# Kernel tuning notes

Measured on AMD Instinct MI355X. Metric: run time of the kernel, lower is better.

Reference implementation:

```python
import jax, jax.numpy as jnp
import numpy as np

T, B = 1024, 128
IDIM, CDIM, N, M = 256, 512, 128, 64


def setup_inputs() -> dict:
    key = jax.random.key(0)
    ks = jax.random.split(key, 10)
    stdev = 5.0 / np.sqrt(IDIM + M + CDIM)  # matches _reset_controller
    u = lambda k, shp: jax.random.uniform(k, shp, jnp.float32, -stdev, stdev)
    return {
        "embs": jax.random.normal(ks[0], (T, B, IDIM), jnp.float32),
        "ilen": T // 2,
        # LSTM controller params (PyTorch layout: [4*cdim, in] / [4*cdim, cdim])
        "w_ih": u(ks[1], (4 * CDIM, IDIM + M)),
        "w_hh": u(ks[2], (4 * CDIM, CDIM)),
        "b_ih": jnp.zeros((4 * CDIM,), jnp.float32),
        "b_hh": jnp.zeros((4 * CDIM,), jnp.float32),
        "h0": jax.random.normal(ks[3], (CDIM,), jnp.float32) * 0.05,
        "c0": jax.random.normal(ks[4], (CDIM,), jnp.float32) * 0.05,
        "r0": jax.random.normal(ks[5], (1, M), jnp.float32) * 0.02,
        # memory head params (concrete subclass): write address / write value / read address
        "W_wa": jax.random.normal(ks[6], (N, CDIM), jnp.float32) * 0.02,
        "b_wa": jnp.zeros((N,), jnp.float32),
        "W_wv": jax.random.normal(ks[7], (M, IDIM), jnp.float32) * 0.02,
        "b_wv": jnp.zeros((M,), jnp.float32),
        "W_ra": jax.random.normal(ks[8], (N, CDIM), jnp.float32) * 0.02,
        "b_ra": jnp.zeros((N,), jnp.float32),
    }


def _forward(embs, w_ih, w_hh, b_ih, b_hh, h0, c0, r0,
             W_wa, b_wa, W_wv, b_wv, W_ra, b_ra, ilen):
    bsz = embs.shape[1]
    h = jnp.broadcast_to(h0, (bsz, CDIM))
    c = jnp.broadcast_to(c0, (bsz, CDIM))
    r = jnp.broadcast_to(r0, (bsz, M))
    mem = jnp.zeros((bsz, N, M), embs.dtype)
    b = b_ih + b_hh

    def step(carry, xt):
        h, c, r, mem = carry
        emb, t = xt  # emb: [B, idim]
        x = jnp.concatenate([emb, r], axis=-1)            # [B, idim+M]
        gates = x @ w_ih.T + h @ w_hh.T + b               # [B, 4*cdim]
        i, f, g, o = jnp.split(gates, 4, axis=-1)         # torch gate order i,f,g,o
        c_new = jax.nn.sigmoid(f) * c + jax.nn.sigmoid(i) * jnp.tanh(g)
        h_new = jax.nn.sigmoid(o) * jnp.tanh(c_new)       # controller_outp
        is_write = t < ilen
        # write(controller_outp, emb): additive write at softmax address
        wa = jax.nn.softmax(h_new @ W_wa.T + b_wa, axis=-1)   # [B, N]
        v = emb @ W_wv.T + b_wv                               # [B, M]
        mem_new = jnp.where(is_write, mem + wa[:, :, None] * v[:, None, :], mem)
        # read(controller_outp): softmax-addressed weighted sum over slots
        ra = jax.nn.softmax(h_new @ W_ra.T + b_ra, axis=-1)   # [B, N]
        r_read = jnp.einsum('bn,bnm->bm', ra, mem_new)        # [B, M]
        r_new = jnp.where(is_write, r, r_read)
        out = jnp.concatenate([h_new, r_new], axis=-1)        # [B, cdim+M]
        return (h_new, c_new, r_new, mem_new), out

    _, os = jax.lax.scan(step, (h, c, r, mem),
                         (embs, jnp.arange(embs.shape[0])))
    return os  # [T, B, cdim+M]


def reference(embs, ilen, w_ih, w_hh, b_ih, b_hh, h0, c0, r0,
              W_wa, b_wa, W_wv, b_wv, W_ra, b_ra):
    return _forward(embs, w_ih, w_hh, b_ih, b_hh, h0, c0, r0,
                    W_wa, b_wa, W_wv, b_wv, W_ra, b_ra, ilen)
```

## Files before the change

### kernel.cpp

```cpp
#include <hip/hip_runtime.h>

typedef _Float16 f16;
typedef __attribute__((ext_vector_type(8))) _Float16 half8;
typedef __attribute__((ext_vector_type(2))) _Float16 half2v;
typedef __attribute__((ext_vector_type(4))) float f32x4;
typedef __attribute__((ext_vector_type(4))) unsigned int u32x4;
typedef unsigned long long u64;

#define TSTEPS 1024

static const size_t OFF_WP   = 0;
static const size_t OFF_BIAS = 3407872;
static const size_t OFF_EMBP = 3416064;
static const size_t OFF_V    = 70524928;
static const size_t OFF_XPRH = 104079360;
static const size_t OFF_MEM  = 104374272;
static const size_t OFF_BAR  = 108568576;
static const size_t OFF_WVP  = 108569600;
static const size_t WS_NEED  = 108602368;


__global__ void marnn_packw(const float* __restrict__ w_ih, const float* __restrict__ w_hh,
                            const float* __restrict__ b_ih, const float* __restrict__ b_hh,
                            f16* __restrict__ WP, float* __restrict__ biasP) {
  int idx = blockIdx.x * 256 + threadIdx.x;
  if (idx < 2048) {
    int j = idx >> 2, g = idx & 3, rg = g * 512 + j;
    biasP[idx] = b_ih[rg] + b_hh[rg];
  }
  if (idx >= 1703936) return;
  int e = idx & 7, l = (idx >> 3) & 63;
  int q = idx >> 9;
  int ks = q % 26; int ntile = q / 26;
  int n = ntile * 16 + (l & 15);
  int k = ks * 32 + (l >> 4) * 8 + e;
  int j2 = n >> 2, g2 = n & 3, rg2 = g2 * 512 + j2;
  float v = (k < 320) ? w_ih[(size_t)rg2 * 320 + k] : w_hh[(size_t)rg2 * 512 + (k - 320)];
  WP[idx] = (f16)v;
}

__global__ void marnn_packwv(const float* __restrict__ W_wv, f16* __restrict__ WVP) {
  int idx = blockIdx.x * 256 + threadIdx.x;
  if (idx >= 16384) return;
  int e = idx & 7, l = (idx >> 3) & 63, ks = (idx >> 9) & 7, nt = idx >> 12;
  int n = nt * 16 + (l & 15);
  int k = ks * 32 + (l >> 4) * 8 + e;
  WVP[idx] = (f16)W_wv[n * 256 + k];
}

__global__ void marnn_packemb(const float* __restrict__ embs, f16* __restrict__ embsP) {
  const long total8 = (long)1024 * 128 * 32;
  const long stride = (long)gridDim.x * blockDim.x;
  for (long i8 = (long)blockIdx.x * blockDim.x + threadIdx.x; i8 < total8; i8 += stride) {
    int bl = (int)(i8 & 15), kc = (int)((i8 >> 4) & 31), bg = (int)((i8 >> 9) & 7);
    long t = i8 >> 12;
    const float* s = embs + ((t * 128) + bg * 16 + bl) * 256 + kc * 8;
    f32x4 a = *(const f32x4*)s, b = *(const f32x4*)(s + 4);
    half8 h;
    h[0]=(f16)a[0]; h[1]=(f16)a[1]; h[2]=(f16)a[2]; h[3]=(f16)a[3];
    h[4]=(f16)b[0]; h[5]=(f16)b[1]; h[6]=(f16)b[2]; h[7]=(f16)b[3];
    *(half8*)(embsP + i8 * 8) = h;
  }
}

__global__ __launch_bounds__(256)
void marnn_vpre(const f16* __restrict__ embsP, const f16* __restrict__ WVP,
                const float* __restrict__ b_wv, float* __restrict__ V) {
  const int tb = blockIdx.x;
  const int wv = threadIdx.x >> 6, l = threadIdx.x & 63;
  half8 bf[8];
  #pragma unroll
  for (int ks = 0; ks < 8; ++ks)
    bf[ks] = *(const half8*)(WVP + ((size_t)(wv * 8 + ks) * 64 + l) * 8);
  const f16* ab = embsP + (size_t)tb * 4096;
  f32x4 acc = {0.f, 0.f, 0.f, 0.f};
  #pragma unroll
  for (int ks = 0; ks < 8; ++ks) {
    half8 af = *(const half8*)(ab + ((size_t)(ks * 4 + (l >> 4)) * 16 + (l & 15)) * 8);
    acc = __builtin_amdgcn_mfma_f32_16x16x32_f16(bf[ks], af, acc, 0, 0, 0);
  }
  const int b = (tb & 7) * 16 + (l & 15);
  const long t = tb >> 3;
  #pragma unroll
  for (int r = 0; r < 4; ++r) {
    int m = wv * 16 + (l >> 4) * 4 + r;
    V[((t * 128) + b) * 64 + m] = acc[r] + b_wv[m];
  }
}

__global__ void marnn_init(const float* __restrict__ h0, const float* __restrict__ r0,
                           f16* __restrict__ XPRH) {
  int idx = blockIdx.x * 256 + threadIdx.x;
  if (idx >= 147456) return;
  int e = idx & 7; int q = idx >> 7; int kcidx = q % 72;
  float v = (kcidx < 8) ? r0[kcidx * 8 + e] : h0[(kcidx - 8) * 8 + e];
  XPRH[idx] = (f16)v;
}


struct __align__(16) MarnnSMem {
  f16  whead[128 * 512];
  char xl[26624];
  char un[4096];
};

__device__ __forceinline__ float marnn_dot8(half8 a, half8 b, float acc) {
#if __has_builtin(__builtin_amdgcn_fdot2)
  half2v a0 = {a[0],a[1]}, a1 = {a[2],a[3]}, a2 = {a[4],a[5]}, a3 = {a[6],a[7]};
  half2v b0 = {b[0],b[1]}, b1 = {b[2],b[3]}, b2 = {b[4],b[5]}, b3 = {b[6],b[7]};
  acc = __builtin_amdgcn_fdot2(a0, b0, acc, false);
  acc = __builtin_amdgcn_fdot2(a1, b1, acc, false);
  acc = __builtin_amdgcn_fdot2(a2, b2, acc, false);
  acc = __builtin_amdgcn_fdot2(a3, b3, acc, false);
#else
  #pragma unroll
  for (int e = 0; e < 8; ++e) acc += (float)a[e] * (float)b[e];
#endif
  return acc;
}

__device__ __forceinline__ float fast_sigmoid(float x) {
  return __builtin_amdgcn_rcpf(1.f + __expf(-x));
}
__device__ __forceinline__ float fast_tanh(float x) {
  return 1.f - 2.f * __builtin_amdgcn_rcpf(1.f + __expf(2.f * x));
}

__device__ __forceinline__ unsigned ld_flag(const unsigned* p) {
  return __hip_atomic_load(p, __ATOMIC_RELAXED, __HIP_MEMORY_SCOPE_AGENT);
}
__device__ __forceinline__ void st_flag(unsigned* p, unsigned v) {
  __hip_atomic_store(p, v, __ATOMIC_RELAXED, __HIP_MEMORY_SCOPE_AGENT);
}
__device__ __forceinline__ u64 ld_llc64(const void* p) {
  return __hip_atomic_load((const u64*)p, __ATOMIC_RELAXED, __HIP_MEMORY_SCOPE_AGENT);
}
__device__ __forceinline__ void st_llc32(void* p, unsigned v) {
  __hip_atomic_store((unsigned*)p, v, __ATOMIC_RELAXED, __HIP_MEMORY_SCOPE_AGENT);
}

__device__ __forceinline__ void poll16(const unsigned* line, unsigned ep) {
  int l = threadIdx.x & 63;
  for (;;) {
    unsigned v = (l < 16) ? ld_flag(line + l) : ep;
    if (__all((int)(v >= ep))) break;
    __builtin_amdgcn_s_sleep(1);
  }
  asm volatile("" ::: "memory");
}

union H2U { f16 f; unsigned short u; };

__global__ __launch_bounds__(512, 1)
void marnn_main(const int* __restrict__ ilen_p, const float* __restrict__ c0,
                const float* __restrict__ r0,
                const float* __restrict__ W_wa, const float* __restrict__ b_wa,
                const float* __restrict__ W_ra, const float* __restrict__ b_ra,
                float* __restrict__ out, char* __restrict__ ws) {
  __shared__ MarnnSMem sm;

  const f16*   WP    = (const f16*)(ws + OFF_WP);
  const float* biasP = (const float*)(ws + OFF_BIAS);
  const f16*   embsP = (const f16*)(ws + OFF_EMBP);
  const float* Vbuf  = (const float*)(ws + OFF_V);
  f16*         XPRH  = (f16*)(ws + OFF_XPRH);
  float*       MEMB  = (float*)(ws + OFF_MEM);
  unsigned*    FLAGS = (unsigned*)(ws + OFF_BAR);

  const int blk = blockIdx.x, tid = threadIdx.x;
  const int wav = tid >> 6, lane = tid & 63;
  const int g = blk & 7, ns = blk >> 3;
  const int ilen = ilen_p[0];
  unsigned* gfh = FLAGS + g * 32;
  unsigned* gfr = gfh + 16;

  half8 bfr[26];
  {
    const f16* wpb = WP + ((size_t)(ns * 8 + wav) * 26) * 512 + lane * 8;
    #pragma unroll
    for (int ks = 0; ks < 26; ++ks) bfr[ks] = *(const half8*)(wpb + ks * 512);
  }

  auto loadWhead = [&](const float* Wsrc) {
    for (int i = tid; i < 8192; i += 512) {
      int n = i >> 6, slot = i & 63;
      const float* s = Wsrc + n * 512 + slot * 8;
      f32x4 a = *(const f32x4*)(s), b2 = *(const f32x4*)(s + 4);
      half8 hv;
      hv[0]=(f16)a[0]; hv[1]=(f16)a[1]; hv[2]=(f16)a[2]; hv[3]=(f16)a[3];
      hv[4]=(f16)b2[0]; hv[5]=(f16)b2[1]; hv[6]=(f16)b2[2]; hv[7]=(f16)b2[3];
      *(half8*)((char*)sm.whead + (n << 10) + (((slot + n) & 63) << 4)) = hv;
    }
  };
  loadWhead(ilen > 0 ? W_wa : W_ra);

  {
    const u32x4* s0 = (const u32x4*)(embsP + ((size_t)0 * 8 + g) * 4096);
    ((u32x4*)sm.xl)[tid] = s0[tid];
    const u32x4* s1 = (const u32x4*)(XPRH + (((size_t)0 * 8 + g) * 72 + 8) * 128);
    u32x4* d1 = (u32x4*)(sm.xl + 10240);
    d1[tid * 2] = s1[tid * 2]; d1[tid * 2 + 1] = s1[tid * 2 + 1];
  }
  __syncthreads();

  const int b_lane = lane & 15, sel = lane >> 4;
  const int jg = ns * 32 + wav * 4 + sel;
  float c = c0[jg];
  const f32x4 bias4 = *(const f32x4*)(biasP + jg * 4);
  const float r0v = (tid < 64) ? r0[tid] : 0.f;
  const int b = g * 16 + ns;

  const float bw0 = b_wa[lane], bw1 = b_wa[lane + 64];
  const float br0 = b_ra[lane], br1 = b_ra[lane + 64];
  const int gn = (wav & 3) * 32 + (lane & 31);
  const int kq = ((wav >> 2) << 1) | (lane >> 5);

  half8 rf0, rf1;
  #pragma unroll
  for (int e = 0; e < 8; ++e) {
    rf0[e] = (f16)r0[sel * 8 + e];
    rf1[e] = (f16)r0[32 + sel * 8 + e];
  }

  for (int t = 0; t < TSTEPS; ++t) {
    const int par = t & 1, nxt = par ^ 1;
    const bool iswrite = (t < ilen);

    u32x4 sa = {0u, 0u, 0u, 0u};
    if (t + 1 < TSTEPS)
      sa = ((const u32x4*)(embsP + (((size_t)(t + 1) * 8) + g) * 4096))[tid];
    f32x4 vv4 = {0.f, 0.f, 0.f, 0.f};
    if (iswrite && wav == 4 && lane < 16)
      vv4 = *(const f32x4*)(Vbuf + ((size_t)t * 128 + b) * 64 + lane * 4);

    f32x4 acc0 = {0.f, 0.f, 0.f, 0.f}, acc1 = {0.f, 0.f, 0.f, 0.f};
    const char* xb = sm.xl + sel * 256 + b_lane * 16;
    #pragma unroll
    for (int ks = 0; ks < 8; ++ks) {
      half8 af = *(const half8*)(xb + ks * 1024);
      if (ks & 1) acc1 = __builtin_amdgcn_mfma_f32_16x16x32_f16(bfr[ks], af, acc1, 0, 0, 0);
      else        acc0 = __builtin_amdgcn_mfma_f32_16x16x32_f16(bfr[ks], af, acc0, 0, 0, 0);
    }
    #pragma unroll
    for (int ks = 10; ks < 26; ++ks) {
      half8 af = *(const half8*)(xb + ks * 1024);
      if (ks & 1) acc1 = __builtin_amdgcn_mfma_f32_16x16x32_f16(bfr[ks], af, acc1, 0, 0, 0);
      else        acc0 = __builtin_amdgcn_mfma_f32_16x16x32_f16(bfr[ks], af, acc0, 0, 0, 0);
    }
    if (t <= ilen) {
      acc0 = __builtin_amdgcn_mfma_f32_16x16x32_f16(bfr[8], rf0, acc0, 0, 0, 0);
      acc1 = __builtin_amdgcn_mfma_f32_16x16x32_f16(bfr[9], rf1, acc1, 0, 0, 0);
    } else {
      if (wav == 0) {
        poll16(gfr, (unsigned)(t - ilen));
        const u64* rp = (const u64*)(XPRH + (((size_t)par * 8 + g) * 72) * 128
                                     + (lane >> 4) * 128 + (lane & 15) * 8);
        union { u64 u[2]; half8 h; } r0u, r1u;
        r0u.u[0] = ld_llc64(rp);       r0u.u[1] = ld_llc64(rp + 1);
        r1u.u[0] = ld_llc64(rp + 128); r1u.u[1] = ld_llc64(rp + 129);
        char* rdst = sm.xl + 8192 + (lane >> 4) * 256 + (lane & 15) * 16;
        *(half8*)rdst = r0u.h;
        *(half8*)(rdst + 1024) = r1u.h;
      }
      __syncthreads();
      acc0 = __builtin_amdgcn_mfma_f32_16x16x32_f16(bfr[8], *(const half8*)(xb + 8 * 1024), acc0, 0, 0, 0);
      acc1 = __builtin_amdgcn_mfma_f32_16x16x32_f16(bfr[9], *(const half8*)(xb + 9 * 1024), acc1, 0, 0, 0);
    }
    const f32x4 acc = acc0 + acc1;

    {
      float si = fast_sigmoid(acc[0] + bias4[0]);
      float sf = fast_sigmoid(acc[1] + bias4[1]);
      float so = fast_sigmoid(acc[3] + bias4[3]);
      c = sf * c + si * fast_tanh(acc[2] + bias4[2]);
      float h = so * fast_tanh(c);
      H2U cv; cv.f = (f16)h;
      unsigned hu = cv.u;
      unsigned pu = __shfl_down(hu, 16, 64);
      if (!(sel & 1))
        st_llc32(&XPRH[(((size_t)nxt * 8 + g) * 72 + 8 + (jg >> 3)) * 128 + b_lane * 8 + (jg & 7)],
                 hu | (pu << 16));
    }
    asm volatile("s_waitcnt vmcnt(0)" ::: "memory");
    __syncthreads();
    if (tid == 0) st_flag(gfh + ns, (unsigned)(t + 1));
    if (wav == 0) poll16(gfh, (unsigned)(t + 1));
    __syncthreads();

    {
      const u64* s1 = (const u64*)(XPRH + (((size_t)nxt * 8 + g) * 72 + 8) * 128);
      u64 hb0 = ld_llc64(s1 + tid * 4 + 0), hb1 = ld_llc64(s1 + tid * 4 + 1);
      u64 hb2 = ld_llc64(s1 + tid * 4 + 2), hb3 = ld_llc64(s1 + tid * 4 + 3);
      ((u32x4*)sm.xl)[tid] = sa;
      u64* d1 = (u64*)(sm.xl + 10240);
      d1[tid * 4 + 0] = hb0; d1[tid * 4 + 1] = hb1;
      d1[tid * 4 + 2] = hb2; d1[tid * 4 + 3] = hb3;
    }
    __syncthreads();

    {
      int ob = tid >> 5, ojj = tid & 31;
      int oj = ns * 32 + ojj;
      f16 hv = *(const f16*)(sm.xl + 10240 + (oj >> 3) * 256 + ob * 16 + (oj & 7) * 2);
      out[(size_t)t * 73728 + (g * 16 + ob) * 576 + oj] = (float)hv;
    }

    if (t == ilen) { loadWhead(W_ra); __syncthreads(); }
    float* pbuf  = (float*)sm.un;
    float* vpart = (float*)(sm.un + 512);
    float* vred  = (float*)(sm.un + 1536);
    float* vsec  = (float*)(sm.un + 3584);
    {
      if (iswrite && wav == 4 && lane < 16) *(f32x4*)(vsec + lane * 4) = vv4;
      const char* wrow = (const char*)sm.whead + (gn << 10);
      const char* hbase = sm.xl + 10240 + ns * 16;
      float av0 = 0.f, av1 = 0.f;
      #pragma unroll
      for (int i = 0; i < 16; i += 2) {
        int s0 = kq * 16 + i;
        av0 = marnn_dot8(*(const half8*)(wrow + (((s0 + gn) & 63) << 4)),
                         *(const half8*)(hbase + s0 * 256), av0);
        av1 = marnn_dot8(*(const half8*)(wrow + (((s0 + 1 + gn) & 63) << 4)),
                         *(const half8*)(hbase + (s0 + 1) * 256), av1);
      }
      float av = av0 + av1;
      av += __shfl_xor(av, 32, 64);
      if (lane < 32) vpart[((wav >> 2) << 7) + gn] = av;
    }
    __syncthreads();
    if (wav == 0) {
      float l0 = vpart[lane] + vpart[128 + lane] + (iswrite ? bw0 : br0);
      float l1 = vpart[64 + lane] + vpart[192 + lane] + (iswrite ? bw1 : br1);
      float mx = fmaxf(l0, l1);
      #pragma unroll
      for (int off = 32; off > 0; off >>= 1) mx = fmaxf(mx, __shfl_xor(mx, off, 64));
      float e0 = __expf(l0 - mx), e1 = __expf(l1 - mx);
      float s = e0 + e1;
      #pragma unroll
      for (int off = 32; off > 0; off >>= 1) s += __shfl_xor(s, off, 64);
      float inv = __builtin_amdgcn_rcpf(s);
      pbuf[lane] = e0 * inv; pbuf[lane + 64] = e1 * inv;
    }
    __syncthreads();
    if (iswrite) {
      float p = pbuf[tid >> 2];
      float* mrow = MEMB + (((size_t)b) * 128 + (tid >> 2)) * 64 + (tid & 3) * 16;
      const float* vv = vsec + (tid & 3) * 16;
      #pragma unroll
      for (int i2 = 0; i2 < 16; i2 += 4) {
        f32x4 mm = *(f32x4*)(mrow + i2);
        f32x4 v4 = *(const f32x4*)(vv + i2);
        mm = mm + p * v4;
        *(f32x4*)(mrow + i2) = mm;
      }
      if (tid < 64)
        out[(size_t)t * 73728 + b * 576 + 512 + tid] = r0v;
    } else {
      const int m = tid & 63;
      const float* mcol = MEMB + (((size_t)b) * 128 + wav * 16) * 64 + m;
      float a0 = 0.f, a1 = 0.f;
      #pragma unroll
      for (int n2 = 0; n2 < 16; n2 += 2) {
        a0 = fmaf(pbuf[wav * 16 + n2],     mcol[n2 * 64],       a0);
        a1 = fmaf(pbuf[wav * 16 + n2 + 1], mcol[(n2 + 1) * 64], a1);
      }
      vred[wav * 64 + m] = a0 + a1;
      __syncthreads();
      if (tid < 64) {
        float rv = 0.f;
        #pragma unroll
        for (int nc = 0; nc < 8; ++nc) rv += vred[nc * 64 + tid];
        H2U cr; cr.f = (f16)rv;
        unsigned ru = cr.u;
        unsigned rp2 = __shfl_down(ru, 1, 64);
        if (!(tid & 1))
          st_llc32(&XPRH[(((size_t)nxt * 8 + g) * 72 + (tid >> 3)) * 128 + ns * 8 + (tid & 7)],
                   ru | (rp2 << 16));
        asm volatile("s_waitcnt vmcnt(0)" ::: "memory");
        if (tid == 0) st_flag(gfr + ns, (unsigned)(t - ilen + 1));
        out[(size_t)t * 73728 + b * 576 + 512 + tid] = rv;
      }
    }
  }
}


extern "C" void kernel_launch(void* const* d_in, const int* in_sizes, int n_in,
                              void* d_out, int out_size, void* d_ws, size_t ws_size,
                              hipStream_t stream) {
  const float* embs = (const float*)d_in[0];
  const int*   ilen = (const int*)d_in[1];
  const float* w_ih = (const float*)d_in[2];
  const float* w_hh = (const float*)d_in[3];
  const float* b_ih = (const float*)d_in[4];
  const float* b_hh = (const float*)d_in[5];
  const float* h0   = (const float*)d_in[6];
  const float* c0   = (const float*)d_in[7];
  const float* r0   = (const float*)d_in[8];
  const float* W_wa = (const float*)d_in[9];
  const float* b_wa = (const float*)d_in[10];
  const float* W_wv = (const float*)d_in[11];
  const float* b_wv = (const float*)d_in[12];
  const float* W_ra = (const float*)d_in[13];
  const float* b_ra = (const float*)d_in[14];
  float* out = (float*)d_out;
  char* ws = (char*)d_ws;
  if (ws_size < WS_NEED) return;

  hipMemsetAsync(ws + OFF_MEM, 0, 4194304, stream);
  hipMemsetAsync(ws + OFF_BAR, 0, 1024, stream);
  marnn_packw<<<6656, 256, 0, stream>>>(w_ih, w_hh, b_ih, b_hh,
                                        (f16*)(ws + OFF_WP), (float*)(ws + OFF_BIAS));
  marnn_packwv<<<64, 256, 0, stream>>>(W_wv, (f16*)(ws + OFF_WVP));
  marnn_packemb<<<2048, 256, 0, stream>>>(embs, (f16*)(ws + OFF_EMBP));
  marnn_vpre<<<8192, 256, 0, stream>>>((const f16*)(ws + OFF_EMBP), (const f16*)(ws + OFF_WVP),
                                       b_wv, (float*)(ws + OFF_V));
  marnn_init<<<576, 256, 0, stream>>>(h0, r0, (f16*)(ws + OFF_XPRH));
  marnn_main<<<128, 512, 0, stream>>>(ilen, c0, r0, W_wa, b_wa, W_ra, b_ra, out, ws);
}
```

Before: 5.250 ms.

## Use per-wave h flags, f16 V, early prefetch and shuffle-broadcast softmax

Each wave now publishes its own readiness flag for the hidden-state exchange, and a wider poll replaces the block barrier that came before the flag store. The next embedding tile and V row are prefetched one step earlier, overlapping the global loads with the barrier wait, and V is stored in f16 to halve its traffic. Every wave now computes the softmax redundantly and broadcasts probabilities with shuffles instead of via shared memory, removing one __syncthreads per step. The trade-offs are more flag polling traffic, lower V precision, and redundant softmax work.

```diff
diff --git a/kernel.cpp b/kernel.cpp
--- a/kernel.cpp
+++ b/kernel.cpp
@@ -13,11 +13,12 @@
 static const size_t OFF_BIAS = 3407872;
 static const size_t OFF_EMBP = 3416064;
 static const size_t OFF_V    = 70524928;
-static const size_t OFF_XPRH = 104079360;
-static const size_t OFF_MEM  = 104374272;
-static const size_t OFF_BAR  = 108568576;
-static const size_t OFF_WVP  = 108569600;
-static const size_t WS_NEED  = 108602368;
+static const size_t OFF_XPRH = 87302144;
+static const size_t OFF_MEM  = 87597056;
+static const size_t OFF_HFLG = 91791360;
+static const size_t OFF_RFLG = 91795456;
+static const size_t OFF_WVP  = 91795968;
+static const size_t WS_NEED  = 91828736;
 
 
 __global__ void marnn_packw(const float* __restrict__ w_ih, const float* __restrict__ w_hh,
@@ -65,7 +66,7 @@
 
 __global__ __launch_bounds__(256)
 void marnn_vpre(const f16* __restrict__ embsP, const f16* __restrict__ WVP,
-                const float* __restrict__ b_wv, float* __restrict__ V) {
+                const float* __restrict__ b_wv, f16* __restrict__ Vh) {
   const int tb = blockIdx.x;
   const int wv = threadIdx.x >> 6, l = threadIdx.x & 63;
   half8 bf[8];
@@ -84,7 +85,7 @@
   #pragma unroll
   for (int r = 0; r < 4; ++r) {
     int m = wv * 16 + (l >> 4) * 4 + r;
-    V[((t * 128) + b) * 64 + m] = acc[r] + b_wv[m];
+    Vh[((t * 128) + b) * 64 + m] = (f16)(acc[r] + b_wv[m]);
   }
 }
 
@@ -148,6 +149,16 @@
   }
   asm volatile("" ::: "memory");
 }
+__device__ __forceinline__ void pollH(const unsigned* base, unsigned ep) {
+  int l = threadIdx.x & 63;
+  for (;;) {
+    unsigned v0 = ld_flag(base + l);
+    unsigned v1 = ld_flag(base + 64 + l);
+    if (__all((int)((v0 >= ep) & (v1 >= ep)))) break;
+    __builtin_amdgcn_s_sleep(1);
+  }
+  asm volatile("" ::: "memory");
+}
 
 union H2U { f16 f; unsigned short u; };
 
@@ -162,17 +173,18 @@
   const f16*   WP    = (const f16*)(ws + OFF_WP);
   const float* biasP = (const float*)(ws + OFF_BIAS);
   const f16*   embsP = (const f16*)(ws + OFF_EMBP);
-  const float* Vbuf  = (const float*)(ws + OFF_V);
+  const f16*   Vh    = (const f16*)(ws + OFF_V);
   f16*         XPRH  = (f16*)(ws + OFF_XPRH);
   float*       MEMB  = (float*)(ws + OFF_MEM);
-  unsigned*    FLAGS = (unsigned*)(ws + OFF_BAR);
+  unsigned*    HFLG  = (unsigned*)(ws + OFF_HFLG);
+  unsigned*    RFLG  = (unsigned*)(ws + OFF_RFLG);
 
   const int blk = blockIdx.x, tid = threadIdx.x;
   const int wav = tid >> 6, lane = tid & 63;
   const int g = blk & 7, ns = blk >> 3;
   const int ilen = ilen_p[0];
-  unsigned* gfh = FLAGS + g * 32;
-  unsigned* gfr = gfh + 16;
+  unsigned* gfh = HFLG + g * 128;
+  unsigned* gfr = RFLG + g * 16;
 
   half8 bfr[26];
   {
@@ -222,16 +234,16 @@
     rf1[e] = (f16)r0[32 + sel * 8 + e];
   }
 
+  u32x4 sa = {0u, 0u, 0u, 0u};
+  if (TSTEPS > 1)
+    sa = ((const u32x4*)(embsP + ((size_t)1 * 8 + g) * 4096))[tid];
+  half8 vh = {};
+  if (ilen > 0 && wav == 4 && lane < 8)
+    vh = *(const half8*)(Vh + ((size_t)0 * 128 + b) * 64 + lane * 8);
+
   for (int t = 0; t < TSTEPS; ++t) {
     const int par = t & 1, nxt = par ^ 1;
     const bool iswrite = (t < ilen);
-
-    u32x4 sa = {0u, 0u, 0u, 0u};
-    if (t + 1 < TSTEPS)
-      sa = ((const u32x4*)(embsP + (((size_t)(t + 1) * 8) + g) * 4096))[tid];
-    f32x4 vv4 = {0.f, 0.f, 0.f, 0.f};
-    if (iswrite && wav == 4 && lane < 16)
-      vv4 = *(const f32x4*)(Vbuf + ((size_t)t * 128 + b) * 64 + lane * 4);
 
     f32x4 acc0 = {0.f, 0.f, 0.f, 0.f}, acc1 = {0.f, 0.f, 0.f, 0.f};
     const char* xb = sm.xl + sel * 256 + b_lane * 16;
@@ -282,9 +294,8 @@
                  hu | (pu << 16));
     }
     asm volatile("s_waitcnt vmcnt(0)" ::: "memory");
-    __syncthreads();
-    if (tid == 0) st_flag(gfh + ns, (unsigned)(t + 1));
-    if (wav == 0) poll16(gfh, (unsigned)(t + 1));
+    if (lane == 0) st_flag(gfh + ns * 8 + wav, (unsigned)(t + 1));
+    if (wav == 0) pollH(gfh, (unsigned)(t + 1));
     __syncthreads();
 
     {
@@ -295,23 +306,31 @@
       u64* d1 = (u64*)(sm.xl + 10240);
       d1[tid * 4 + 0] = hb0; d1[tid * 4 + 1] = hb1;
       d1[tid * 4 + 2] = hb2; d1[tid * 4 + 3] = hb3;
+      if (t + 2 < TSTEPS)
+        sa = ((const u32x4*)(embsP + (((size_t)(t + 2) * 8) + g) * 4096))[tid];
     }
     __syncthreads();
 
     {
       int ob = tid >> 5, ojj = tid & 31;
       int oj = ns * 32 + ojj;
-      f16 hv = *(const f16*)(sm.xl + 10240 + (oj >> 3) * 256 + ob * 16 + (oj & 7) * 2);
-      out[(size_t)t * 73728 + (g * 16 + ob) * 576 + oj] = (float)hv;
+      f16 hv2 = *(const f16*)(sm.xl + 10240 + (oj >> 3) * 256 + ob * 16 + (oj & 7) * 2);
+      out[(size_t)t * 73728 + (g * 16 + ob) * 576 + oj] = (float)hv2;
     }
 
     if (t == ilen) { loadWhead(W_ra); __syncthreads(); }
-    float* pbuf  = (float*)sm.un;
-    float* vpart = (float*)(sm.un + 512);
-    float* vred  = (float*)(sm.un + 1536);
-    float* vsec  = (float*)(sm.un + 3584);
+    float* vpart = (float*)sm.un;
+    float* vred  = (float*)(sm.un + 1024);
+    float* vsec  = (float*)(sm.un + 3072);
     {
-      if (iswrite && wav == 4 && lane < 16) *(f32x4*)(vsec + lane * 4) = vv4;
+      if (iswrite && wav == 4 && lane < 8) {
+        f32x4 lo = {(float)vh[0], (float)vh[1], (float)vh[2], (float)vh[3]};
+        f32x4 hi = {(float)vh[4], (float)vh[5], (float)vh[6], (float)vh[7]};
+        *(f32x4*)(vsec + lane * 8) = lo;
+        *(f32x4*)(vsec + lane * 8 + 4) = hi;
+        if (t + 1 < ilen)
+          vh = *(const half8*)(Vh + ((size_t)(t + 1) * 128 + b) * 64 + lane * 8);
+      }
       const char* wrow = (const char*)sm.whead + (gn << 10);
       const char* hbase = sm.xl + 10240 + ns * 16;
       float av0 = 0.f, av1 = 0.f;
@@ -328,7 +347,9 @@
       if (lane < 32) vpart[((wav >> 2) << 7) + gn] = av;
     }
     __syncthreads();
-    if (wav == 0) {
+
+    float p0, p1;
+    {
       float l0 = vpart[lane] + vpart[128 + lane] + (iswrite ? bw0 : br0);
       float l1 = vpart[64 + lane] + vpart[192 + lane] + (iswrite ? bw1 : br1);
       float mx = fmaxf(l0, l1);
@@ -339,12 +360,15 @@
       #pragma unroll
       for (int off = 32; off > 0; off >>= 1) s += __shfl_xor(s, off, 64);
       float inv = __builtin_amdgcn_rcpf(s);
-      pbuf[lane] = e0 * inv; pbuf[lane + 64] = e1 * inv;
-    }
-    __syncthreads();
+      p0 = e0 * inv; p1 = e1 * inv;
+    }
+
     if (iswrite) {
-      float p = pbuf[tid >> 2];
-      float* mrow = MEMB + (((size_t)b) * 128 + (tid >> 2)) * 64 + (tid & 3) * 16;
+      int n = tid >> 2;
+      float pA = __shfl(p0, n & 63, 64);
+      float pB = __shfl(p1, n & 63, 64);
+      float p = (n < 64) ? pA : pB;
+      float* mrow = MEMB + (((size_t)b) * 128 + n) * 64 + (tid & 3) * 16;
       const float* vv = vsec + (tid & 3) * 16;
       #pragma unroll
       for (int i2 = 0; i2 < 16; i2 += 4) {
@@ -361,8 +385,10 @@
       float a0 = 0.f, a1 = 0.f;
       #pragma unroll
       for (int n2 = 0; n2 < 16; n2 += 2) {
-        a0 = fmaf(pbuf[wav * 16 + n2],     mcol[n2 * 64],       a0);
-        a1 = fmaf(pbuf[wav * 16 + n2 + 1], mcol[(n2 + 1) * 64], a1);
+        float q0 = __shfl((wav < 4) ? p0 : p1, (wav * 16 + n2) & 63, 64);
+        float q1 = __shfl((wav < 4) ? p0 : p1, (wav * 16 + n2 + 1) & 63, 64);
+        a0 = fmaf(q0, mcol[n2 * 64], a0);
+        a1 = fmaf(q1, mcol[(n2 + 1) * 64], a1);
       }
       vred[wav * 64 + m] = a0 + a1;
       __syncthreads();
@@ -408,13 +434,13 @@
   if (ws_size < WS_NEED) return;
 
   hipMemsetAsync(ws + OFF_MEM, 0, 4194304, stream);
-  hipMemsetAsync(ws + OFF_BAR, 0, 1024, stream);
+  hipMemsetAsync(ws + OFF_HFLG, 0, 4608, stream);
   marnn_packw<<<6656, 256, 0, stream>>>(w_ih, w_hh, b_ih, b_hh,
                                         (f16*)(ws + OFF_WP), (float*)(ws + OFF_BIAS));
   marnn_packwv<<<64, 256, 0, stream>>>(W_wv, (f16*)(ws + OFF_WVP));
   marnn_packemb<<<2048, 256, 0, stream>>>(embs, (f16*)(ws + OFF_EMBP));
   marnn_vpre<<<8192, 256, 0, stream>>>((const f16*)(ws + OFF_EMBP), (const f16*)(ws + OFF_WVP),
-                                       b_wv, (float*)(ws + OFF_V));
+                                       b_wv, (f16*)(ws + OFF_V));
   marnn_init<<<576, 256, 0, stream>>>(h0, r0, (f16*)(ws + OFF_XPRH));
   marnn_main<<<128, 512, 0, stream>>>(ilen, c0, r0, W_wa, b_wa, W_ra, b_ra, out, ws);
 }
```

Result: slower. 7.664 ms (+46.0%).
